# Performance work log

Measured on AMD Instinct MI355X. Metric: run time of the kernel, lower is better.

Reference implementation:

```python
import jax, jax.numpy as jnp
from jax import lax
import numpy as np

ALPHA = 1.0
GAMMA = 1e-6
KBLK = 64  # codebook block size for the L1 NN search scan


def setup_inputs() -> dict:
    key = jax.random.key(0)
    ks = jax.random.split(key, 6)
    B, T, C, F, D, K = 8, 1024, 32, 256, 128, 512
    return {
        "X": jax.random.normal(ks[0], (B, T, C), jnp.float32),
        "H": jax.random.normal(ks[1], (B, D, T), jnp.float32),
        "M": jax.random.normal(ks[2], (D, K), jnp.float32),
        "Hdec": jax.random.normal(ks[3], (B, T, F), jnp.float32),
        "W": jax.random.normal(ks[4], (C, F), jnp.float32) * 0.05,
        "w_d": jax.random.normal(ks[5], (C,), jnp.float32) * 0.05,
    }


def _memory_loss(H, M):
    # H: [B, D, T], M: [D, K]
    Ht = jnp.transpose(H, (0, 2, 1))            # [B, T, D]
    MT = M.T                                     # [K, D] codewords
    K, D = MT.shape
    nblk = K // KBLK
    blocks = MT.reshape(nblk, KBLK, D)
    bases = jnp.arange(nblk, dtype=jnp.int32) * KBLK

    def step(carry, blk_base):
        best_d, best_i = carry
        blk, base = blk_base
        # L1 distance to this block of codewords: [B, T, KBLK]
        d = jnp.sum(jnp.abs(Ht[:, :, None, :] - blk[None, None, :, :]), axis=-1)
        bd = jnp.min(d, axis=-1)
        bi = jnp.argmin(d, axis=-1).astype(jnp.int32) + base
        upd = bd < best_d  # strict < keeps the first (lowest-index) argmin, as torch does
        return (jnp.where(upd, bd, best_d), jnp.where(upd, bi, best_i)), None

    init = (jnp.full(Ht.shape[:2], jnp.inf, Ht.dtype),
            jnp.zeros(Ht.shape[:2], jnp.int32))
    (_, best_i), _ = lax.scan(step, init, (blocks, bases))

    Zt = MT[best_i]  # [B, T, D] gathered nearest codewords
    sg = lax.stop_gradient
    # sum of per-(b,d) squared L2 norms over T == total squared sum
    diffs = jnp.sum((sg(Ht) - Zt) ** 2) + jnp.sum((Ht - sg(Zt)) ** 2)
    return diffs / float(np.prod(H.shape))


def reference(X, H, M, Hdec, W, w_d):
    # decoder last layer + discriminator head (needed for adaptive weight grads)
    def rec_loss(w):
        Xhat = jnp.einsum('btf,cf->btc', Hdec, w)
        return jnp.mean((Xhat - X) ** 2)

    def d_loss(w):
        Xhat = jnp.einsum('btf,cf->btc', Hdec, w)
        return -jnp.mean(Xhat @ w_d)

    loss_rec = rec_loss(W)
    loss_d = d_loss(W)
    loss_m = _memory_loss(H, M)

    g_rec = jax.grad(rec_loss)(W)
    g_d = jax.grad(d_loss)(W)
    lmbda = lax.stop_gradient(
        jnp.linalg.norm(g_rec) / (jnp.linalg.norm(g_d) + GAMMA))

    return loss_rec + ALPHA * loss_m + lmbda * loss_d
```

## Files before the change

### kernel.cpp

```cpp
#include <hip/hip_runtime.h>
#include <hip/hip_bf16.h>
#include <math.h>

#define N_POS 8192
#define D_DIM 128
#define K_DIM 512
#define C_DIM 32
#define F_DIM 256
#define NKT   4
#define GREC_COLS 8448
#define L2_BLOCKS 388

__device__ __forceinline__ float block_reduce_256(float v) {
    __shared__ float sbuf[4];
    __syncthreads();
#pragma unroll
    for (int off = 32; off > 0; off >>= 1) v += __shfl_down(v, off);
    const int lane = threadIdx.x & 63;
    const int w    = threadIdx.x >> 6;
    if (lane == 0) sbuf[w] = v;
    __syncthreads();
    return (threadIdx.x == 0) ? (sbuf[0] + sbuf[1] + sbuf[2] + sbuf[3]) : 0.f;
}

__global__ __launch_bounds__(256)
void fused_l1(const float* __restrict__ H, const float* __restrict__ M,
              const float* __restrict__ Hdec, const float* __restrict__ W,
              const float* __restrict__ X, const float* __restrict__ w_d,
              float* __restrict__ MT, float* __restrict__ pd,
              int* __restrict__ pi, float* __restrict__ pp,
              float* __restrict__ accum) {
    __shared__ __align__(16) char smem_raw[49152];
    const int tid = threadIdx.x;

    if (blockIdx.x < 256) {
        float* hT = (float*)smem_raw;
        float* mT = hT + 4096;
        float* rd = mT + 4096;
        int*   ri = (int*)(rd + 2048);

        const int ptile = blockIdx.x >> 2;
        const int ktile = blockIdx.x & 3;
        const int pos0  = ptile << 7;
        const int b     = pos0 >> 10;
        const int t0    = pos0 & 1023;
        const int k0    = ktile << 7;
        const float* Hb = H + (b << 17) + t0;

        const int tq = (tid & 31) << 2;
        const int dq = tid >> 5;
        const int p4 = (tid & 15) << 2;
        const int q4 = (tid >> 4) << 2;

        float acc[8][8];
#pragma unroll
        for (int i = 0; i < 8; ++i)
#pragma unroll
            for (int j = 0; j < 8; ++j) acc[i][j] = 0.f;

        for (int ch = 0; ch < 4; ++ch) {
            const int d0 = ch << 5;
            __syncthreads();
#pragma unroll
            for (int p = 0; p < 4; ++p) {
                const int d = (p << 3) + dq;
                *(float4*)(hT + (d << 7) + tq) =
                    *(const float4*)(Hb + ((size_t)(d0 + d) << 10) + tq);
                *(float4*)(mT + (d << 7) + tq) =
                    *(const float4*)(M + (size_t)(d0 + d) * K_DIM + k0 + tq);
            }
            __syncthreads();
#pragma unroll 2
            for (int d = 0; d < 32; ++d) {
                const float4 ha = *(const float4*)(hT + (d << 7) + p4);
                const float4 hc = *(const float4*)(hT + (d << 7) + 64 + p4);
                const float4 ma = *(const float4*)(mT + (d << 7) + q4);
                const float4 mc = *(const float4*)(mT + (d << 7) + 64 + q4);
                const float hh[8] = {ha.x, ha.y, ha.z, ha.w, hc.x, hc.y, hc.z, hc.w};
                const float mm[8] = {ma.x, ma.y, ma.z, ma.w, mc.x, mc.y, mc.z, mc.w};
#pragma unroll
                for (int i = 0; i < 8; ++i)
#pragma unroll
                    for (int j = 0; j < 8; ++j)
                        acc[i][j] += fabsf(hh[i] - mm[j]);
            }
        }

#pragma unroll
        for (int i = 0; i < 8; ++i) {
            const int pl = (i < 4) ? (p4 + i) : (64 + p4 + i - 4);
            float bd = acc[i][0];
            int   bj = 0;
#pragma unroll
            for (int j = 1; j < 8; ++j)
                if (acc[i][j] < bd) { bd = acc[i][j]; bj = j; }
            const int bk = k0 + ((bj < 4) ? (q4 + bj) : (64 + q4 + bj - 4));
            rd[(tid >> 4) * 128 + pl] = bd;
            ri[(tid >> 4) * 128 + pl] = bk;
        }
        __syncthreads();

        if (tid < 128) {
            float bd = rd[tid];
            int   bi = ri[tid];
#pragma unroll
            for (int q = 1; q < 16; ++q) {
                const float d = rd[q * 128 + tid];
                const int   k = ri[q * 128 + tid];
                if (d < bd || (d == bd && k < bi)) { bd = d; bi = k; }
            }
            pd[ktile * N_POS + pos0 + tid] = bd;
            pi[ktile * N_POS + pos0 + tid] = bi;
        }
    } else {
        float* Wl = (float*)smem_raw;
        float* El = Wl + C_DIM * 260;
        const int xb  = blockIdx.x - 256;
        const int bt0 = xb << 5;

        if (xb < 64) {
            const int d0 = xb << 1;
            const int d  = d0 + (tid >> 7);
            const int k  = (tid & 127) << 2;
#pragma unroll
            for (int j = 0; j < 4; ++j)
                MT[(size_t)(k + j) * D_DIM + d] = M[(size_t)d * K_DIM + k + j];
        }

#pragma unroll
        for (int it = 0; it < 8; ++it) {
            const int i = it * 1024 + tid * 4;
            const float4 v = *(const float4*)(W + i);
            *(float4*)(Wl + (i >> 8) * 260 + (i & 255)) = v;
        }
        __syncthreads();

        const int c  = tid & 31;
        const int rg = tid >> 5;
        const int r0 = bt0 + rg, r1 = r0 + 8, r2 = r0 + 16, r3 = r0 + 24;

        float a0 = 0.f, a1 = 0.f, a2 = 0.f, a3 = 0.f;
#pragma unroll 4
        for (int f0 = 0; f0 < F_DIM; f0 += 4) {
            const float4 w4 = *(const float4*)(Wl + c * 260 + f0);
            const float4 h0 = *(const float4*)(Hdec + (size_t)r0 * F_DIM + f0);
            const float4 h1 = *(const float4*)(Hdec + (size_t)r1 * F_DIM + f0);
            const float4 h2 = *(const float4*)(Hdec + (size_t)r2 * F_DIM + f0);
            const float4 h3 = *(const float4*)(Hdec + (size_t)r3 * F_DIM + f0);
            a0 += h0.x * w4.x + h0.y * w4.y + h0.z * w4.z + h0.w * w4.w;
            a1 += h1.x * w4.x + h1.y * w4.y + h1.z * w4.z + h1.w * w4.w;
            a2 += h2.x * w4.x + h2.y * w4.y + h2.z * w4.z + h2.w * w4.w;
            a3 += h3.x * w4.x + h3.y * w4.y + h3.z * w4.z + h3.w * w4.w;
        }

        const float wd = w_d[c];
        const float e0 = a0 - X[(size_t)r0 * C_DIM + c];
        const float e1 = a1 - X[(size_t)r1 * C_DIM + c];
        const float e2 = a2 - X[(size_t)r2 * C_DIM + c];
        const float e3 = a3 - X[(size_t)r3 * C_DIM + c];
        El[(rg)      * 32 + c] = e0;
        El[(rg + 8)  * 32 + c] = e1;
        El[(rg + 16) * 32 + c] = e2;
        El[(rg + 24) * 32 + c] = e3;
        const float sse = e0 * e0 + e1 * e1 + e2 * e2 + e3 * e3;
        const float dp  = (a0 + a1 + a2 + a3) * wd;
        const float rA = block_reduce_256(sse);
        if (tid == 0) atomicAdd(accum + 0, rA);
        const float rB = block_reduce_256(dp);
        if (tid == 0) atomicAdd(accum + 1, rB);
        __syncthreads();

        const int f = tid;
        float gacc[C_DIM];
#pragma unroll
        for (int cc = 0; cc < C_DIM; ++cc) gacc[cc] = 0.f;
        float sf = 0.f;
#pragma unroll 1
        for (int i = 0; i < 32; ++i) {
            const float hd = Hdec[(size_t)(bt0 + i) * F_DIM + f];
            sf += hd;
#pragma unroll
            for (int c4 = 0; c4 < 8; ++c4) {
                const float4 e4 = *(const float4*)(El + i * 32 + c4 * 4);
                gacc[c4 * 4 + 0] += e4.x * hd;
                gacc[c4 * 4 + 1] += e4.y * hd;
                gacc[c4 * 4 + 2] += e4.z * hd;
                gacc[c4 * 4 + 3] += e4.w * hd;
            }
        }
        float* o = pp + (size_t)xb * GREC_COLS;
#pragma unroll
        for (int cc = 0; cc < C_DIM; ++cc) o[cc * F_DIM + f] = gacc[cc];
        o[8192 + f] = sf;
    }
}

__global__ __launch_bounds__(256)
void fused_l2(const float* __restrict__ H, const float* __restrict__ MT,
              const float* __restrict__ pd, const int* __restrict__ pi,
              const float* __restrict__ pp, const float* __restrict__ w_d,
              float* __restrict__ accum, float* __restrict__ out) {
    const int tid = threadIdx.x;
    if (blockIdx.x < 256) {
        const int bx = blockIdx.x & 31;
        const int by = blockIdx.x >> 5;
        const int pos = bx * 256 + tid;
        const int b = pos >> 10;
        const int t = pos & 1023;

        float bd = INFINITY;
        int   bi = 0x7fffffff;
#pragma unroll
        for (int p = 0; p < NKT; ++p) {
            const float d = pd[p * N_POS + pos];
            const int   k = pi[p * N_POS + pos];
            if (d < bd || (d == bd && k < bi)) { bd = d; bi = k; }
        }

        const int d0 = by * 16;
        const float* Hb = H + (b << 17) + t + (d0 << 10);
        const float* z  = MT + (size_t)bi * D_DIM + d0;
        const float4 z0 = *(const float4*)(z);
        const float4 z1 = *(const float4*)(z + 4);
        const float4 z2 = *(const float4*)(z + 8);
        const float4 z3 = *(const float4*)(z + 12);
        float s0 = 0.f, s1 = 0.f, s2 = 0.f, s3 = 0.f;
        float e;
        e = Hb[0  << 10] - z0.x; s0 += e * e;
        e = Hb[1  << 10] - z0.y; s1 += e * e;
        e = Hb[2  << 10] - z0.z; s2 += e * e;
        e = Hb[3  << 10] - z0.w; s3 += e * e;
        e = Hb[4  << 10] - z1.x; s0 += e * e;
        e = Hb[5  << 10] - z1.y; s1 += e * e;
        e = Hb[6  << 10] - z1.z; s2 += e * e;
        e = Hb[7  << 10] - z1.w; s3 += e * e;
        e = Hb[8  << 10] - z2.x; s0 += e * e;
        e = Hb[9  << 10] - z2.y; s1 += e * e;
        e = Hb[10 << 10] - z2.z; s2 += e * e;
        e = Hb[11 << 10] - z2.w; s3 += e * e;
        e = Hb[12 << 10] - z3.x; s0 += e * e;
        e = Hb[13 << 10] - z3.y; s1 += e * e;
        e = Hb[14 << 10] - z3.z; s2 += e * e;
        e = Hb[15 << 10] - z3.w; s3 += e * e;
        const float r = block_reduce_256((s0 + s1) + (s2 + s3));
        if (tid == 0) atomicAdd(accum + 2, r);
    } else {
        const int g = blockIdx.x - 256;
        const int col = (g < 128) ? (g * 64 + (tid & 63))
                                  : (8192 + (g - 128) * 64 + (tid & 63));
        const int pc  = tid >> 6;
        const float* base = pp + (size_t)(pc * 64) * GREC_COLS + col;
        float s = 0.f;
#pragma unroll 8
        for (int p = 0; p < 64; ++p) s += base[(size_t)p * GREC_COLS];
        __shared__ float red[4][64];
        red[pc][tid & 63] = s;
        __syncthreads();
        if (tid < 64) {
            const float tot = red[0][tid] + red[1][tid] +
                              red[2][tid] + red[3][tid];
            float v = tot * tot;
#pragma unroll
            for (int off = 32; off > 0; off >>= 1) v += __shfl_down(v, off);
            if (tid == 0)
                atomicAdd(accum + ((g >= 128) ? 4 : 3), v);
        }
    }

    __shared__ int is_last;
    if (tid == 0) {
        __threadfence();
        unsigned int* cnt = (unsigned int*)(accum + 5);
        is_last = (atomicAdd(cnt, 1u) == L2_BLOCKS - 1);
    }
    __syncthreads();
    if (is_last && tid < 64) {
        float wd2 = (tid < C_DIM) ? w_d[tid] * w_d[tid] : 0.f;
#pragma unroll
        for (int off = 32; off > 0; off >>= 1) wd2 += __shfl_down(wd2, off);
        if (tid == 0) {
            __threadfence();
            const float sse_rec = atomicAdd(accum + 0, 0.f);
            const float dsum    = atomicAdd(accum + 1, 0.f);
            const float sse_mem = atomicAdd(accum + 2, 0.f);
            const float g2      = atomicAdd(accum + 3, 0.f);
            const float s2      = atomicAdd(accum + 4, 0.f);
            const float loss_rec = sse_rec / 262144.f;
            const float loss_d   = -dsum / 8192.f;
            const float loss_m   = 2.f * sse_mem / 1048576.f;
            const float ngrec    = (2.f / 262144.f) * sqrtf(g2);
            const float ngd      = sqrtf(wd2 * s2) / 8192.f;
            const float lmbda    = ngrec / (ngd + 1e-6f);
            out[0] = loss_rec + loss_m + lmbda * loss_d;
        }
    }
}

extern "C" void kernel_launch(void* const* d_in, const int* in_sizes, int n_in,
                              void* d_out, int out_size, void* d_ws, size_t ws_size,
                              hipStream_t stream) {
    const float* X    = (const float*)d_in[0];
    const float* H    = (const float*)d_in[1];
    const float* M    = (const float*)d_in[2];
    const float* Hdec = (const float*)d_in[3];
    const float* W    = (const float*)d_in[4];
    const float* w_d  = (const float*)d_in[5];

    float* ws    = (float*)d_ws;
    float* MT    = ws;
    float* accum = ws + 65536;
    float* pd    = ws + 65552;
    int*   pi    = (int*)(ws + 98320);
    float* pp    = ws + 131088;

    hipMemsetAsync(accum, 0, 16 * sizeof(float), stream);
    fused_l1<<<512,       256, 0, stream>>>(H, M, Hdec, W, X, w_d,
                                            MT, pd, pi, pp, accum);
    fused_l2<<<L2_BLOCKS, 256, 0, stream>>>(H, MT, pd, pi, pp, w_d,
                                            accum, (float*)d_out);
}
```

Measured before the change: 132.9 us.

## Fuse both stages into one kernel with last-block reductions and packed argmin

Merges the two launches into a single kernel. The last k-tile block per position tile finalizes the argmin and computes the memory loss directly from M, and the last block overall computes the final scalar. The NN tile shrinks to 64 positions with 512 blocks, and distance and index are packed into a 64-bit key so a min gives the lowest-index tie-break. The gradient partial buffer is replaced by atomicAdds from 32 larger X/grad blocks. This removes a launch, the MT transpose and the partial-sum pass, at the cost of more global atomics, uncoalesced M column reads, and a serial tail in the last block.

New measurement: 294.0 us. 121% more time.

```diff
diff --git a/kernel.cpp b/kernel.cpp
--- a/kernel.cpp
+++ b/kernel.cpp
@@ -1,5 +1,4 @@
 #include <hip/hip_runtime.h>
-#include <hip/hip_bf16.h>
 #include <math.h>
 
 #define N_POS 8192
@@ -7,9 +6,14 @@
 #define K_DIM 512
 #define C_DIM 32
 #define F_DIM 256
-#define NKT   4
-#define GREC_COLS 8448
-#define L2_BLOCKS 388
+
+#define PT 64
+#define KW 128
+#define NN_BLOCKS 512
+#define XG_BLOCKS 32
+#define GRID (NN_BLOCKS + XG_BLOCKS)
+
+#define ZWS_FLOATS 8592
 
 __device__ __forceinline__ float block_reduce_256(float v) {
     __shared__ float sbuf[4];
@@ -23,63 +27,72 @@
     return (threadIdx.x == 0) ? (sbuf[0] + sbuf[1] + sbuf[2] + sbuf[3]) : 0.f;
 }
 
-__global__ __launch_bounds__(256)
-void fused_l1(const float* __restrict__ H, const float* __restrict__ M,
-              const float* __restrict__ Hdec, const float* __restrict__ W,
-              const float* __restrict__ X, const float* __restrict__ w_d,
-              float* __restrict__ MT, float* __restrict__ pd,
-              int* __restrict__ pi, float* __restrict__ pp,
-              float* __restrict__ accum) {
-    __shared__ __align__(16) char smem_raw[49152];
+__global__ __launch_bounds__(256, 2)
+void fused_all(const float* __restrict__ H, const float* __restrict__ M,
+               const float* __restrict__ Hdec, const float* __restrict__ W,
+               const float* __restrict__ X, const float* __restrict__ w_d,
+               float* __restrict__ zws,
+               unsigned long long* __restrict__ pd64,
+               float* __restrict__ out) {
+    __shared__ __align__(16) char smem[49664];
+    float* accum = zws;
+    unsigned int* ptile_cnt = (unsigned int*)(zws + 8);
+    unsigned int* gcnt      = (unsigned int*)(zws + 136);
+    float* g_rec = zws + 144;
+    float* S     = zws + 8336;
     const int tid = threadIdx.x;
 
-    if (blockIdx.x < 256) {
-        float* hT = (float*)smem_raw;
-        float* mT = hT + 4096;
-        float* rd = mT + 4096;
-        int*   ri = (int*)(rd + 2048);
+    if (blockIdx.x < NN_BLOCKS) {
+        float* hT = (float*)smem;
+        float* mT = hT + 2048;
+        unsigned long long* red64 = (unsigned long long*)(smem + 24576);
 
         const int ptile = blockIdx.x >> 2;
         const int ktile = blockIdx.x & 3;
-        const int pos0  = ptile << 7;
+        const int pos0  = ptile * PT;
         const int b     = pos0 >> 10;
         const int t0    = pos0 & 1023;
-        const int k0    = ktile << 7;
+        const int k0    = ktile * KW;
         const float* Hb = H + (b << 17) + t0;
 
-        const int tq = (tid & 31) << 2;
-        const int dq = tid >> 5;
         const int p4 = (tid & 15) << 2;
-        const int q4 = (tid >> 4) << 2;
-
-        float acc[8][8];
-#pragma unroll
-        for (int i = 0; i < 8; ++i)
+        const int q8 = (tid >> 4) << 3;
+
+        float acc[4][8];
+#pragma unroll
+        for (int i = 0; i < 4; ++i)
 #pragma unroll
             for (int j = 0; j < 8; ++j) acc[i][j] = 0.f;
 
         for (int ch = 0; ch < 4; ++ch) {
             const int d0 = ch << 5;
             __syncthreads();
-#pragma unroll
-            for (int p = 0; p < 4; ++p) {
-                const int d = (p << 3) + dq;
-                *(float4*)(hT + (d << 7) + tq) =
-                    *(const float4*)(Hb + ((size_t)(d0 + d) << 10) + tq);
-                *(float4*)(mT + (d << 7) + tq) =
-                    *(const float4*)(M + (size_t)(d0 + d) * K_DIM + k0 + tq);
+            {
+                int idx = tid * 4;
+#pragma unroll
+                for (int it = 0; it < 2; ++it, idx += 1024) {
+                    const int d = idx >> 6, cc = idx & 63;
+                    *(float4*)(hT + idx) =
+                        *(const float4*)(Hb + ((size_t)(d0 + d) << 10) + cc);
+                }
+                idx = tid * 4;
+#pragma unroll
+                for (int it = 0; it < 4; ++it, idx += 1024) {
+                    const int d = idx >> 7, cc = idx & 127;
+                    *(float4*)(mT + idx) =
+                        *(const float4*)(M + (size_t)(d0 + d) * K_DIM + k0 + cc);
+                }
             }
             __syncthreads();
 #pragma unroll 2
             for (int d = 0; d < 32; ++d) {
-                const float4 ha = *(const float4*)(hT + (d << 7) + p4);
-                const float4 hc = *(const float4*)(hT + (d << 7) + 64 + p4);
-                const float4 ma = *(const float4*)(mT + (d << 7) + q4);
-                const float4 mc = *(const float4*)(mT + (d << 7) + 64 + q4);
-                const float hh[8] = {ha.x, ha.y, ha.z, ha.w, hc.x, hc.y, hc.z, hc.w};
-                const float mm[8] = {ma.x, ma.y, ma.z, ma.w, mc.x, mc.y, mc.z, mc.w};
-#pragma unroll
-                for (int i = 0; i < 8; ++i)
+                const float4 h4 = *(const float4*)(hT + (d << 6) + p4);
+                const float4 m0 = *(const float4*)(mT + (d << 7) + q8);
+                const float4 m1 = *(const float4*)(mT + (d << 7) + q8 + 4);
+                const float hh[4] = {h4.x, h4.y, h4.z, h4.w};
+                const float mm[8] = {m0.x, m0.y, m0.z, m0.w, m1.x, m1.y, m1.z, m1.w};
+#pragma unroll
+                for (int i = 0; i < 4; ++i)
 #pragma unroll
                     for (int j = 0; j < 8; ++j)
                         acc[i][j] += fabsf(hh[i] - mm[j]);
@@ -87,45 +100,63 @@
         }
 
 #pragma unroll
-        for (int i = 0; i < 8; ++i) {
-            const int pl = (i < 4) ? (p4 + i) : (64 + p4 + i - 4);
+        for (int i = 0; i < 4; ++i) {
             float bd = acc[i][0];
             int   bj = 0;
 #pragma unroll
             for (int j = 1; j < 8; ++j)
                 if (acc[i][j] < bd) { bd = acc[i][j]; bj = j; }
-            const int bk = k0 + ((bj < 4) ? (q4 + bj) : (64 + q4 + bj - 4));
-            rd[(tid >> 4) * 128 + pl] = bd;
-            ri[(tid >> 4) * 128 + pl] = bk;
+            const unsigned int bk = (unsigned int)(k0 + q8 + bj);
+            red64[(tid >> 4) * PT + p4 + i] =
+                ((unsigned long long)__float_as_uint(bd) << 32) | bk;
         }
         __syncthreads();
-
-        if (tid < 128) {
-            float bd = rd[tid];
-            int   bi = ri[tid];
-#pragma unroll
-            for (int q = 1; q < 16; ++q) {
-                const float d = rd[q * 128 + tid];
-                const int   k = ri[q * 128 + tid];
-                if (d < bd || (d == bd && k < bi)) { bd = d; bi = k; }
-            }
-            pd[ktile * N_POS + pos0 + tid] = bd;
-            pi[ktile * N_POS + pos0 + tid] = bi;
+        if (tid < PT) {
+            unsigned long long best = red64[tid];
+#pragma unroll
+            for (int g = 1; g < 16; ++g) {
+                const unsigned long long w = red64[g * PT + tid];
+                if (w < best) best = w;
+            }
+            pd64[ktile * N_POS + pos0 + tid] = best;
+        }
+        __threadfence();
+        __syncthreads();
+        __shared__ int lastp;
+        if (tid == 0) lastp = (atomicAdd(&ptile_cnt[ptile], 1u) == 3u);
+        __syncthreads();
+        if (lastp) {
+            int* bi_l = (int*)smem;
+            if (tid < PT) {
+                unsigned long long best = ~0ull;
+#pragma unroll
+                for (int p = 0; p < 4; ++p) {
+                    const unsigned long long w = __hip_atomic_load(
+                        pd64 + p * N_POS + pos0 + tid,
+                        __ATOMIC_RELAXED, __HIP_MEMORY_SCOPE_AGENT);
+                    if (w < best) best = w;
+                }
+                bi_l[tid] = (int)(unsigned int)(best & 0xffffffffu);
+            }
+            __syncthreads();
+            const int pl = tid & 63;
+            const int dh = tid >> 6;
+            const int bi = bi_l[pl];
+            const float* Hp = H + (b << 17) + t0 + pl;
+            float s = 0.f;
+#pragma unroll 8
+            for (int d = dh * 32; d < dh * 32 + 32; ++d) {
+                const float e = Hp[(size_t)d << 10] - M[(size_t)d * K_DIM + bi];
+                s += e * e;
+            }
+            const float r = block_reduce_256(s);
+            if (tid == 0) atomicAdd(accum + 2, r);
         }
     } else {
-        float* Wl = (float*)smem_raw;
+        float* Wl = (float*)smem;
         float* El = Wl + C_DIM * 260;
-        const int xb  = blockIdx.x - 256;
-        const int bt0 = xb << 5;
-
-        if (xb < 64) {
-            const int d0 = xb << 1;
-            const int d  = d0 + (tid >> 7);
-            const int k  = (tid & 127) << 2;
-#pragma unroll
-            for (int j = 0; j < 4; ++j)
-                MT[(size_t)(k + j) * D_DIM + d] = M[(size_t)d * K_DIM + k + j];
-        }
+        const int xb  = blockIdx.x - NN_BLOCKS;
+        const int bt0 = xb << 8;
 
 #pragma unroll
         for (int it = 0; it < 8; ++it) {
@@ -133,163 +164,93 @@
             const float4 v = *(const float4*)(W + i);
             *(float4*)(Wl + (i >> 8) * 260 + (i & 255)) = v;
         }
-        __syncthreads();
-
         const int c  = tid & 31;
         const int rg = tid >> 5;
-        const int r0 = bt0 + rg, r1 = r0 + 8, r2 = r0 + 16, r3 = r0 + 24;
-
-        float a0 = 0.f, a1 = 0.f, a2 = 0.f, a3 = 0.f;
-#pragma unroll 4
-        for (int f0 = 0; f0 < F_DIM; f0 += 4) {
-            const float4 w4 = *(const float4*)(Wl + c * 260 + f0);
-            const float4 h0 = *(const float4*)(Hdec + (size_t)r0 * F_DIM + f0);
-            const float4 h1 = *(const float4*)(Hdec + (size_t)r1 * F_DIM + f0);
-            const float4 h2 = *(const float4*)(Hdec + (size_t)r2 * F_DIM + f0);
-            const float4 h3 = *(const float4*)(Hdec + (size_t)r3 * F_DIM + f0);
-            a0 += h0.x * w4.x + h0.y * w4.y + h0.z * w4.z + h0.w * w4.w;
-            a1 += h1.x * w4.x + h1.y * w4.y + h1.z * w4.z + h1.w * w4.w;
-            a2 += h2.x * w4.x + h2.y * w4.y + h2.z * w4.z + h2.w * w4.w;
-            a3 += h3.x * w4.x + h3.y * w4.y + h3.z * w4.z + h3.w * w4.w;
-        }
-
         const float wd = w_d[c];
-        const float e0 = a0 - X[(size_t)r0 * C_DIM + c];
-        const float e1 = a1 - X[(size_t)r1 * C_DIM + c];
-        const float e2 = a2 - X[(size_t)r2 * C_DIM + c];
-        const float e3 = a3 - X[(size_t)r3 * C_DIM + c];
-        El[(rg)      * 32 + c] = e0;
-        El[(rg + 8)  * 32 + c] = e1;
-        El[(rg + 16) * 32 + c] = e2;
-        El[(rg + 24) * 32 + c] = e3;
-        const float sse = e0 * e0 + e1 * e1 + e2 * e2 + e3 * e3;
-        const float dp  = (a0 + a1 + a2 + a3) * wd;
+        float gacc[C_DIM];
+#pragma unroll
+        for (int cc = 0; cc < C_DIM; ++cc) gacc[cc] = 0.f;
+        float sf = 0.f, sse = 0.f, dp = 0.f;
+
+        for (int pass = 0; pass < 2; ++pass) {
+            const int rb = bt0 + pass * 128;
+            __syncthreads();
+            float a[16];
+#pragma unroll
+            for (int j = 0; j < 16; ++j) a[j] = 0.f;
+#pragma unroll 2
+            for (int f0 = 0; f0 < F_DIM; f0 += 4) {
+                const float4 w4 = *(const float4*)(Wl + c * 260 + f0);
+#pragma unroll
+                for (int j = 0; j < 16; ++j) {
+                    const float4 h4 = *(const float4*)(
+                        Hdec + (size_t)(rb + rg + 8 * j) * F_DIM + f0);
+                    a[j] += h4.x * w4.x + h4.y * w4.y + h4.z * w4.z + h4.w * w4.w;
+                }
+            }
+#pragma unroll
+            for (int j = 0; j < 16; ++j) {
+                const int r = rb + rg + 8 * j;
+                const float e = a[j] - X[(size_t)r * C_DIM + c];
+                El[(rg + 8 * j) * C_DIM + c] = e;
+                sse += e * e;
+                dp  += a[j] * wd;
+            }
+            __syncthreads();
+#pragma unroll 1
+            for (int i = 0; i < 128; ++i) {
+                const float hd = Hdec[(size_t)(rb + i) * F_DIM + tid];
+                sf += hd;
+#pragma unroll
+                for (int c4 = 0; c4 < 8; ++c4) {
+                    const float4 e4 = *(const float4*)(El + i * C_DIM + c4 * 4);
+                    gacc[c4 * 4 + 0] += e4.x * hd;
+                    gacc[c4 * 4 + 1] += e4.y * hd;
+                    gacc[c4 * 4 + 2] += e4.z * hd;
+                    gacc[c4 * 4 + 3] += e4.w * hd;
+                }
+            }
+        }
+#pragma unroll 1
+        for (int cc = 0; cc < C_DIM; ++cc)
+            atomicAdd(&g_rec[cc * F_DIM + tid], gacc[cc]);
+        atomicAdd(&S[tid], sf);
         const float rA = block_reduce_256(sse);
         if (tid == 0) atomicAdd(accum + 0, rA);
         const float rB = block_reduce_256(dp);
         if (tid == 0) atomicAdd(accum + 1, rB);
-        __syncthreads();
-
-        const int f = tid;
-        float gacc[C_DIM];
-#pragma unroll
-        for (int cc = 0; cc < C_DIM; ++cc) gacc[cc] = 0.f;
-        float sf = 0.f;
-#pragma unroll 1
-        for (int i = 0; i < 32; ++i) {
-            const float hd = Hdec[(size_t)(bt0 + i) * F_DIM + f];
-            sf += hd;
-#pragma unroll
-            for (int c4 = 0; c4 < 8; ++c4) {
-                const float4 e4 = *(const float4*)(El + i * 32 + c4 * 4);
-                gacc[c4 * 4 + 0] += e4.x * hd;
-                gacc[c4 * 4 + 1] += e4.y * hd;
-                gacc[c4 * 4 + 2] += e4.z * hd;
-                gacc[c4 * 4 + 3] += e4.w * hd;
-            }
-        }
-        float* o = pp + (size_t)xb * GREC_COLS;
-#pragma unroll
-        for (int cc = 0; cc < C_DIM; ++cc) o[cc * F_DIM + f] = gacc[cc];
-        o[8192 + f] = sf;
     }
-}
-
-__global__ __launch_bounds__(256)
-void fused_l2(const float* __restrict__ H, const float* __restrict__ MT,
-              const float* __restrict__ pd, const int* __restrict__ pi,
-              const float* __restrict__ pp, const float* __restrict__ w_d,
-              float* __restrict__ accum, float* __restrict__ out) {
-    const int tid = threadIdx.x;
-    if (blockIdx.x < 256) {
-        const int bx = blockIdx.x & 31;
-        const int by = blockIdx.x >> 5;
-        const int pos = bx * 256 + tid;
-        const int b = pos >> 10;
-        const int t = pos & 1023;
-
-        float bd = INFINITY;
-        int   bi = 0x7fffffff;
-#pragma unroll
-        for (int p = 0; p < NKT; ++p) {
-            const float d = pd[p * N_POS + pos];
-            const int   k = pi[p * N_POS + pos];
-            if (d < bd || (d == bd && k < bi)) { bd = d; bi = k; }
-        }
-
-        const int d0 = by * 16;
-        const float* Hb = H + (b << 17) + t + (d0 << 10);
-        const float* z  = MT + (size_t)bi * D_DIM + d0;
-        const float4 z0 = *(const float4*)(z);
-        const float4 z1 = *(const float4*)(z + 4);
-        const float4 z2 = *(const float4*)(z + 8);
-        const float4 z3 = *(const float4*)(z + 12);
-        float s0 = 0.f, s1 = 0.f, s2 = 0.f, s3 = 0.f;
-        float e;
-        e = Hb[0  << 10] - z0.x; s0 += e * e;
-        e = Hb[1  << 10] - z0.y; s1 += e * e;
-        e = Hb[2  << 10] - z0.z; s2 += e * e;
-        e = Hb[3  << 10] - z0.w; s3 += e * e;
-        e = Hb[4  << 10] - z1.x; s0 += e * e;
-        e = Hb[5  << 10] - z1.y; s1 += e * e;
-        e = Hb[6  << 10] - z1.z; s2 += e * e;
-        e = Hb[7  << 10] - z1.w; s3 += e * e;
-        e = Hb[8  << 10] - z2.x; s0 += e * e;
-        e = Hb[9  << 10] - z2.y; s1 += e * e;
-        e = Hb[10 << 10] - z2.z; s2 += e * e;
-        e = Hb[11 << 10] - z2.w; s3 += e * e;
-        e = Hb[12 << 10] - z3.x; s0 += e * e;
-        e = Hb[13 << 10] - z3.y; s1 += e * e;
-        e = Hb[14 << 10] - z3.z; s2 += e * e;
-        e = Hb[15 << 10] - z3.w; s3 += e * e;
-        const float r = block_reduce_256((s0 + s1) + (s2 + s3));
-        if (tid == 0) atomicAdd(accum + 2, r);
-    } else {
-        const int g = blockIdx.x - 256;
-        const int col = (g < 128) ? (g * 64 + (tid & 63))
-                                  : (8192 + (g - 128) * 64 + (tid & 63));
-        const int pc  = tid >> 6;
-        const float* base = pp + (size_t)(pc * 64) * GREC_COLS + col;
-        float s = 0.f;
-#pragma unroll 8
-        for (int p = 0; p < 64; ++p) s += base[(size_t)p * GREC_COLS];
-        __shared__ float red[4][64];
-        red[pc][tid & 63] = s;
-        __syncthreads();
+
+    __shared__ int lastg;
+    __threadfence();
+    __syncthreads();
+    if (tid == 0) lastg = (atomicAdd(gcnt, 1u) == (unsigned)(GRID - 1));
+    __syncthreads();
+    if (lastg) {
+        float g2 = 0.f;
+        for (int i = tid; i < 8192; i += 256) {
+            const float v = __hip_atomic_load(g_rec + i, __ATOMIC_RELAXED,
+                                              __HIP_MEMORY_SCOPE_AGENT);
+            g2 += v * v;
+        }
+        const float rg2 = block_reduce_256(g2);
+        const float vS = __hip_atomic_load(S + tid, __ATOMIC_RELAXED,
+                                           __HIP_MEMORY_SCOPE_AGENT);
+        const float rs2 = block_reduce_256(vS * vS);
+        float wd2 = (tid < C_DIM) ? w_d[tid] * w_d[tid] : 0.f;
         if (tid < 64) {
-            const float tot = red[0][tid] + red[1][tid] +
-                              red[2][tid] + red[3][tid];
-            float v = tot * tot;
-#pragma unroll
-            for (int off = 32; off > 0; off >>= 1) v += __shfl_down(v, off);
-            if (tid == 0)
-                atomicAdd(accum + ((g >= 128) ? 4 : 3), v);
-        }
-    }
-
-    __shared__ int is_last;
-    if (tid == 0) {
-        __threadfence();
-        unsigned int* cnt = (unsigned int*)(accum + 5);
-        is_last = (atomicAdd(cnt, 1u) == L2_BLOCKS - 1);
-    }
-    __syncthreads();
-    if (is_last && tid < 64) {
-        float wd2 = (tid < C_DIM) ? w_d[tid] * w_d[tid] : 0.f;
-#pragma unroll
-        for (int off = 32; off > 0; off >>= 1) wd2 += __shfl_down(wd2, off);
+#pragma unroll
+            for (int off = 32; off > 0; off >>= 1) wd2 += __shfl_down(wd2, off);
+        }
         if (tid == 0) {
-            __threadfence();
             const float sse_rec = atomicAdd(accum + 0, 0.f);
             const float dsum    = atomicAdd(accum + 1, 0.f);
             const float sse_mem = atomicAdd(accum + 2, 0.f);
-            const float g2      = atomicAdd(accum + 3, 0.f);
-            const float s2      = atomicAdd(accum + 4, 0.f);
             const float loss_rec = sse_rec / 262144.f;
             const float loss_d   = -dsum / 8192.f;
             const float loss_m   = 2.f * sse_mem / 1048576.f;
-            const float ngrec    = (2.f / 262144.f) * sqrtf(g2);
-            const float ngd      = sqrtf(wd2 * s2) / 8192.f;
+            const float ngrec    = (2.f / 262144.f) * sqrtf(rg2);
+            const float ngd      = sqrtf(wd2 * rs2) / 8192.f;
             const float lmbda    = ngrec / (ngd + 1e-6f);
             out[0] = loss_rec + loss_m + lmbda * loss_d;
         }
@@ -306,16 +267,10 @@
     const float* W    = (const float*)d_in[4];
     const float* w_d  = (const float*)d_in[5];
 
-    float* ws    = (float*)d_ws;
-    float* MT    = ws;
-    float* accum = ws + 65536;
-    float* pd    = ws + 65552;
-    int*   pi    = (int*)(ws + 98320);
-    float* pp    = ws + 131088;
-
-    hipMemsetAsync(accum, 0, 16 * sizeof(float), stream);
-    fused_l1<<<512,       256, 0, stream>>>(H, M, Hdec, W, X, w_d,
-                                            MT, pd, pi, pp, accum);
-    fused_l2<<<L2_BLOCKS, 256, 0, stream>>>(H, MT, pd, pi, pp, w_d,
-                                            accum, (float*)d_out);
+    float* zws = (float*)d_ws;
+    unsigned long long* pd64 = (unsigned long long*)(zws + ZWS_FLOATS);
+
+    hipMemsetAsync(zws, 0, ZWS_FLOATS * sizeof(float), stream);
+    fused_all<<<GRID, 256, 0, stream>>>(H, M, Hdec, W, X, w_d,
+                                        zws, pd64, (float*)d_out);
 }
```
